# Optimization experiments

Measured on AMD Instinct MI355X. Metric: run time of the kernel, lower is better.

The kernel has to match this reference:

```python
import jax, jax.numpy as jnp
import numpy as np

EPS = 1e-5
NUM_HEADS = 8

def _inorm(x):
    # InstanceNorm1d (affine=False): normalize over last (length) axis per (B, C)
    m = x.mean(axis=-1, keepdims=True)
    v = x.var(axis=-1, keepdims=True)  # biased variance, as torch instance norm
    return (x - m) * jax.lax.rsqrt(v + EPS)

def setup_inputs() -> dict:
    key = jax.random.key(0)
    ks = jax.random.split(key, 12)
    B, Nl, HW = 4, 1024, 4096
    Cl, Cv, Ck, Cval, Cout = 512, 512, 256, 256, 256
    w = lambda k, shape: (jax.random.normal(k, shape, jnp.float32) * 0.02)
    return {
        "l": jax.random.normal(ks[0], (B, Nl, Cl), jnp.float32),
        "x": jax.random.normal(ks[1], (B, HW, Cv), jnp.float32),
        "Wq": w(ks[2], (Ck, Cl)),   "bq": w(ks[3], (Ck,)),
        "Wk": w(ks[4], (Ck, Cv)),   "bk": w(ks[5], (Ck,)),
        "Wv": w(ks[6], (Cval, Cv)), "bv": w(ks[7], (Cval,)),
        "Ww": w(ks[8], (Cout, Cval)), "bw": w(ks[9], (Cout,)),
    }

def reference(l, x, Wq, bq, Wk, bk, Wv, bv, Ww, bw):
    H = NUM_HEADS
    Ck = Wq.shape[0]
    Cv = Wv.shape[0]
    dk, dv = Ck // H, Cv // H
    B, Nl, _ = l.shape
    HW = x.shape[1]

    # 1x1 Conv1d == per-position linear
    q = jnp.einsum('blc,kc->blk', l, Wq) + bq                     # [B, Nl, Ck]
    k = jnp.einsum('bnc,kc->bkn', x, Wk) + bk[None, :, None]      # [B, Ck, HW]
    k = _inorm(k)                                                  # InstanceNorm over HW
    v = jnp.einsum('bnc,kc->bkn', x, Wv) + bv[None, :, None]      # [B, Cv, HW]

    q = q.reshape(B, Nl, H, dk).transpose(0, 2, 1, 3)             # [B, H, Nl, dk]
    k = k.reshape(B, H, dk, HW)                                   # [B, H, dk, HW]
    v = v.reshape(B, H, dv, HW)                                   # [B, H, dv, HW]

    sim = jnp.einsum('bhld,bhdn->bhln', q, k) * (Ck ** -0.5)      # [B, H, Nl, HW]
    att = jax.nn.softmax(sim, axis=-1)
    out = jnp.einsum('bhln,bhdn->bhld', att, v)                   # [B, H, Nl, dv]

    out = out.transpose(0, 2, 1, 3).reshape(B, Nl, Cv)            # [B, Nl, Cv]
    out = jnp.einsum('blc,oc->bol', out, Ww) + bw[None, :, None]  # [B, Cout, Nl]
    out = _inorm(out)                                              # InstanceNorm over Nl
    return out.transpose(0, 2, 1)                                  # [B, Nl, Cout]
```

## Files before the change

kernel.cpp:

```cpp
#include <hip/hip_runtime.h>

constexpr int Bn = 4, NL = 1024, HWn = 4096, NH = 8;

typedef __attribute__((ext_vector_type(8))) short bf16x8;
typedef __attribute__((ext_vector_type(4))) float f32x4;
#define MFMA16 __builtin_amdgcn_mfma_f32_16x16x32_bf16

extern "C" __device__ float __ocml_native_exp2_f32(float);

__device__ __forceinline__ float b2f(unsigned short u) {
  union { unsigned int i; float f; } x; x.i = ((unsigned int)u) << 16; return x.f;
}
__device__ __forceinline__ unsigned short f2b(float f) {
  union { float f; unsigned int i; } x; x.f = f;
  unsigned int r = x.i + 0x7fffu + ((x.i >> 16) & 1u);
  return (unsigned short)(r >> 16);
}

__device__ __forceinline__ void async_load16(const unsigned short* g, unsigned short* l) {
  __builtin_amdgcn_global_load_lds(
      (const __attribute__((address_space(1))) unsigned int*)g,
      (__attribute__((address_space(3))) unsigned int*)l, 16, 0, 0);
}

__global__ __launch_bounds__(256) void conv_bf16(const float* __restrict__ src,
    unsigned short* __restrict__ dst, int n)
{
  int i = (blockIdx.x * 256 + threadIdx.x) * 4;
  if (i < n) {
    float4 v = *(const float4*)(src + i);
    ushort4 o; o.x = f2b(v.x); o.y = f2b(v.y); o.z = f2b(v.z); o.w = f2b(v.w);
    *(ushort4*)(dst + i) = o;
  }
}

__global__ __launch_bounds__(256) void conv_w4(const float* __restrict__ Wk,
    const float* __restrict__ Wv, const float* __restrict__ Wq,
    const float* __restrict__ Ww,
    unsigned short* __restrict__ wkb, unsigned short* __restrict__ wvb,
    unsigned short* __restrict__ wqb,
    unsigned short* __restrict__ wwh, unsigned short* __restrict__ wwl)
{
  int i = (blockIdx.x * 256 + threadIdx.x) * 4;
  if (blockIdx.y == 3) {
    if (i >= 65536) return;
    float4 v = *(const float4*)(Ww + i);
    ushort4 hi, lo;
    hi.x = f2b(v.x); lo.x = f2b(v.x - b2f(hi.x));
    hi.y = f2b(v.y); lo.y = f2b(v.y - b2f(hi.y));
    hi.z = f2b(v.z); lo.z = f2b(v.z - b2f(hi.z));
    hi.w = f2b(v.w); lo.w = f2b(v.w - b2f(hi.w));
    *(ushort4*)(wwh + i) = hi;
    *(ushort4*)(wwl + i) = lo;
    return;
  }
  const float* src = blockIdx.y == 0 ? Wk : (blockIdx.y == 1 ? Wv : Wq);
  unsigned short* dst = blockIdx.y == 0 ? wkb : (blockIdx.y == 1 ? wvb : wqb);
  float4 v = *(const float4*)(src + i);
  ushort4 o; o.x = f2b(v.x); o.y = f2b(v.y); o.z = f2b(v.z); o.w = f2b(v.w);
  *(ushort4*)(dst + i) = o;
}

__global__ __launch_bounds__(256, 3) void gemm128(
    const unsigned short* __restrict__ xbf, const unsigned short* __restrict__ lbf,
    const unsigned short* __restrict__ wkb, const unsigned short* __restrict__ wvb,
    const unsigned short* __restrict__ wqb,
    const float* __restrict__ bk, const float* __restrict__ bv, const float* __restrict__ bq,
    unsigned short* __restrict__ khb, unsigned short* __restrict__ vhb,
    unsigned short* __restrict__ qbuf,
    float* __restrict__ ksum, float* __restrict__ kss, float* __restrict__ vcs)
{
  __shared__ unsigned short As[2][4096];
  __shared__ unsigned short Bs[2][4096];
  const int id = blockIdx.x;
  const int mode = id < 256 ? 0 : (id < 512 ? 1 : 2);
  const int local = id - (mode == 0 ? 0 : (mode == 1 ? 256 : 512));
  const int rb = local >> 1, cb = local & 1;
  const int m0 = rb * 128, n0 = cb * 128;
  const unsigned short* A = (mode == 2) ? lbf : xbf;
  const unsigned short* W = (mode == 0) ? wkb : (mode == 1 ? wvb : wqb);
  const float* bias = (mode == 0) ? bk : (mode == 1 ? bv : bq);

  const int tid = threadIdx.x, w = tid >> 6, lane = tid & 63;
  const int quad = lane >> 4, l15 = lane & 15;
  const int wr = w >> 1, wc = w & 1;

  const int p0 = tid, p1 = tid + 256;
  const int am0 = p0 >> 2, ak0 = (p0 & 3) * 8;
  const int am1 = p1 >> 2, ak1 = (p1 & 3) * 8;

  f32x4 acc[4][4];
#pragma unroll
  for (int i = 0; i < 4; ++i)
#pragma unroll
    for (int j = 0; j < 4; ++j) acc[i][j] = (f32x4){0.f, 0.f, 0.f, 0.f};

  async_load16(A + (size_t)(m0 + am0) * 512 + ak0, &As[0][p0 * 8]);
  async_load16(A + (size_t)(m0 + am1) * 512 + ak1, &As[0][p1 * 8]);
  async_load16(W + (size_t)(n0 + am0) * 512 + ak0, &Bs[0][p0 * 8]);
  async_load16(W + (size_t)(n0 + am1) * 512 + ak1, &Bs[0][p1 * 8]);

  for (int kt = 0; kt < 16; ++kt) {
    const int cur = kt & 1;
    __syncthreads();
    if (kt < 15) {
      int k0 = (kt + 1) * 32;
      async_load16(A + (size_t)(m0 + am0) * 512 + k0 + ak0, &As[cur ^ 1][p0 * 8]);
      async_load16(A + (size_t)(m0 + am1) * 512 + k0 + ak1, &As[cur ^ 1][p1 * 8]);
      async_load16(W + (size_t)(n0 + am0) * 512 + k0 + ak0, &Bs[cur ^ 1][p0 * 8]);
      async_load16(W + (size_t)(n0 + am1) * 512 + k0 + ak1, &Bs[cur ^ 1][p1 * 8]);
    }
    bf16x8 af[4], bf[4];
#pragma unroll
    for (int fr = 0; fr < 4; ++fr)
      af[fr] = *(const bf16x8*)&As[cur][(wr * 64 + fr * 16 + l15) * 32 + quad * 8];
#pragma unroll
    for (int fc = 0; fc < 4; ++fc)
      bf[fc] = *(const bf16x8*)&Bs[cur][(wc * 64 + fc * 16 + l15) * 32 + quad * 8];
#pragma unroll
    for (int fr = 0; fr < 4; ++fr)
#pragma unroll
      for (int fc = 0; fc < 4; ++fc)
        acc[fr][fc] = MFMA16(af[fr], bf[fc], acc[fr][fc], 0, 0, 0);
  }

  float bb[4];
#pragma unroll
  for (int fc = 0; fc < 4; ++fc) bb[fc] = bias[n0 + wc * 64 + fc * 16 + l15];

  if (mode != 2) {
    const int b = m0 >> 12;
    const int seg = (m0 & 4095) >> 9;
#pragma unroll
    for (int fc = 0; fc < 4; ++fc) {
      float s = 0.f, ssq = 0.f;
#pragma unroll
      for (int fr = 0; fr < 4; ++fr)
#pragma unroll
        for (int r = 0; r < 4; ++r) {
          float v = acc[fr][fc][r] + bb[fc];
          s += v; ssq += v * v;
        }
      s += __shfl_xor(s, 16); s += __shfl_xor(s, 32);
      if (mode == 0) {
        ssq += __shfl_xor(ssq, 16); ssq += __shfl_xor(ssq, 32);
        if (quad == 0) {
          int col = n0 + wc * 64 + fc * 16 + l15;
          atomicAdd(&ksum[b * 256 + col], s);
          atomicAdd(&kss[b * 256 + col], ssq);
        }
      } else if (quad == 0) {
        int col = n0 + wc * 64 + fc * 16 + l15;
        atomicAdd(&vcs[seg * 1024 + b * 256 + col], s);
      }
    }
  }

  unsigned short* dst = (mode == 0) ? khb : (mode == 1 ? vhb : qbuf);
#pragma unroll
  for (int fr = 0; fr < 4; ++fr) {
#pragma unroll
    for (int fc = 0; fc < 4; ++fc) {
      int col = n0 + wc * 64 + fc * 16 + l15;
#pragma unroll
      for (int r = 0; r < 4; ++r) {
        int row = m0 + wr * 64 + fr * 16 + quad * 4 + r;
        unsigned short val = f2b(acc[fr][fc][r] + bb[fc]);
        if (mode == 2) {
          dst[(size_t)row * 256 + col] = val;
        } else {
          int b = row >> 12, n = row & 4095, h = col >> 5, d = col & 31;
          dst[((size_t)(b * 8 + h) * 4096 + n) * 32 + d] = val;
        }
      }
    }
  }
}

__global__ __launch_bounds__(256) void kfinal(const float* __restrict__ ksum,
    const float* __restrict__ kss, float* __restrict__ krstd)
{
  int i = blockIdx.x * 256 + threadIdx.x;
  float m = ksum[i] * (1.f / 4096.f);
  float var = kss[i] * (1.f / 4096.f) - m * m;
  krstd[i] = rsqrtf(var + 1e-5f);
}

__global__ __launch_bounds__(256) void vpack(const unsigned short* __restrict__ vh,
    unsigned short* __restrict__ vfrag)
{
  __shared__ unsigned short vt[256][42];
  const int bh = blockIdx.x >> 4, slab = blockIdx.x & 15;
  const unsigned short* src = vh + ((size_t)bh * 4096 + slab * 256) * 32;
  const int t = threadIdx.x;
#pragma unroll
  for (int i = 0; i < 4; ++i) {
    int p = i * 256 + t;
    int n = p >> 2, piece = p & 3;
    uint4 v = *(const uint4*)(src + (size_t)n * 32 + piece * 8);
    unsigned int* lrow = (unsigned int*)&vt[n][piece * 8];
    lrow[0] = v.x; lrow[1] = v.y; lrow[2] = v.z; lrow[3] = v.w;
  }
  __syncthreads();
#pragma unroll
  for (int i = 0; i < 4; ++i) {
    int op = i * 256 + t;
    int lanep = op & 63, rest = op >> 6;
    int dvt = rest & 1, kh2 = (rest >> 1) & 1, chunkl = rest >> 2;
    int lq = lanep >> 4, ll = lanep & 15;
    unsigned short o[8];
#pragma unroll
    for (int j = 0; j < 8; ++j) {
      int kappa = kh2 * 32 + lq * 8 + j;
      int nloc = (kappa >> 2) + 16 * (kappa & 3);
      o[j] = vt[chunkl * 64 + nloc][dvt * 16 + ll];
    }
    size_t dst = ((((size_t)bh * 64 + slab * 4 + chunkl) * 2 + kh2) * 2 + dvt) * 512 + lanep * 8;
    *(bf16x8*)(vfrag + dst) = *(const bf16x8*)o;
  }
}

__global__ __launch_bounds__(256, 4) void attn8(const unsigned short* __restrict__ qbuf,
    const unsigned short* __restrict__ khb, const unsigned short* __restrict__ vfrag,
    const float* __restrict__ krstd, const float* __restrict__ vcs,
    float* __restrict__ po, float* __restrict__ pd)
{
  const int bh = blockIdx.x, b = bh >> 3, h = bh & 7;
  const int lsuper = blockIdx.y, quarter = blockIdx.z;
  const int tid = threadIdx.x, w = tid >> 6, lane = tid & 63;
  const int quad = lane >> 4, l15 = lane & 15;

  __shared__ unsigned short kb_s[2][2048];
  __shared__ unsigned short vb_s[2][2048];
  __shared__ unsigned short ps[4][2][16][64];

  bf16x8 qa[2];
  {
    float fold[8];
    const float* rp = krstd + bh * 32 + quad * 8;
#pragma unroll
    for (int j = 0; j < 8; ++j) fold[j] = rp[j] * (0.0625f * 1.44269504f);
#pragma unroll
    for (int lf = 0; lf < 2; ++lf) {
      int l = lsuper * 128 + w * 32 + lf * 16 + l15;
      bf16x8 qr = *(const bf16x8*)(qbuf + ((size_t)(b * NL + l)) * 256 + h * 32 + quad * 8);
      const unsigned short* qq = (const unsigned short*)&qr;
      unsigned short tmp[8];
#pragma unroll
      for (int j = 0; j < 8; ++j) tmp[j] = f2b(b2f(qq[j]) * fold[j]);
      qa[lf] = *(const bf16x8*)tmp;
    }
  }

  float drow[2][4];
  f32x4 acc[2][2];
#pragma unroll
  for (int lf = 0; lf < 2; ++lf) {
#pragma unroll
    for (int r = 0; r < 4; ++r) drow[lf][r] = 0.f;
    acc[lf][0] = (f32x4){0.f,0.f,0.f,0.f};
    acc[lf][1] = (f32x4){0.f,0.f,0.f,0.f};
  }

  const unsigned short* kcbase = khb + (size_t)bh * 131072 + (size_t)quarter * 1024 * 32;
  const unsigned short* vcbase = vfrag + (size_t)bh * 131072 + (size_t)quarter * 16 * 2048;

  async_load16(kcbase + tid * 8, &kb_s[0][tid * 8]);
  async_load16(vcbase + tid * 8, &vb_s[0][tid * 8]);

  unsigned short* psw = &ps[w][0][0][0];
  const unsigned rdswz = (unsigned)((l15 & 7) << 4);

  for (int c = 0; c < 16; ++c) {
    const int cur = c & 1;
    __syncthreads();
    if (c < 15) {
      async_load16(kcbase + (c + 1) * 2048 + tid * 8, &kb_s[cur ^ 1][tid * 8]);
      async_load16(vcbase + (c + 1) * 2048 + tid * 8, &vb_s[cur ^ 1][tid * 8]);
    }

    bf16x8 kb[4];
#pragma unroll
    for (int t = 0; t < 4; ++t)
      kb[t] = *(const bf16x8*)&kb_s[cur][(t * 16 + l15) * 32 + quad * 8];
    bf16x8 vb[4];
#pragma unroll
    for (int i = 0; i < 4; ++i)
      vb[i] = *(const bf16x8*)&vb_s[cur][i * 512 + lane * 8];

    const f32x4 z = (f32x4){0.f,0.f,0.f,0.f};
#pragma unroll
    for (int lf = 0; lf < 2; ++lf) {
      f32x4 sv[4];
#pragma unroll
      for (int t = 0; t < 4; ++t) sv[t] = MFMA16(qa[lf], kb[t], z, 0, 0, 0);
#pragma unroll
      for (int r = 0; r < 4; ++r) {
        float x0 = __ocml_native_exp2_f32(sv[0][r]);
        float x1 = __ocml_native_exp2_f32(sv[1][r]);
        float x2 = __ocml_native_exp2_f32(sv[2][r]);
        float x3 = __ocml_native_exp2_f32(sv[3][r]);
        drow[lf][r] += (x0 + x1) + (x2 + x3);
        unsigned pk0, pk1;
        asm("v_cvt_pk_bf16_f32 %0, %1, %2" : "=v"(pk0) : "v"(x0 - 1.0f), "v"(x1 - 1.0f));
        asm("v_cvt_pk_bf16_f32 %0, %1, %2" : "=v"(pk1) : "v"(x2 - 1.0f), "v"(x3 - 1.0f));
        const int row = quad * 4 + r;
        unsigned off = (unsigned)((l15 * 8) ^ ((row & 7) << 4));
        uint2 pk; pk.x = pk0; pk.y = pk1;
        *(uint2*)((char*)(psw + lf * 1024 + row * 64) + off) = pk;
      }
      asm volatile("s_waitcnt lgkmcnt(0)" ::: "memory");
#pragma unroll
      for (int kh2 = 0; kh2 < 2; ++kh2) {
        unsigned off = (unsigned)((kh2 * 64 + quad * 16) ^ rdswz);
        bf16x8 pa = *(const bf16x8*)((const char*)(psw + lf * 1024 + l15 * 64) + off);
        acc[lf][0] = MFMA16(pa, vb[kh2 * 2 + 0], acc[lf][0], 0, 0, 0);
        acc[lf][1] = MFMA16(pa, vb[kh2 * 2 + 1], acc[lf][1], 0, 0, 0);
      }
    }
  }

  const float* vc0 = vcs + (quarter * 2) * 1024 + bh * 32;
  const float* vc1 = vc0 + 1024;
  float cs0 = vc0[l15] + vc1[l15];
  float cs1 = vc0[16 + l15] + vc1[16 + l15];
#pragma unroll
  for (int lf = 0; lf < 2; ++lf)
#pragma unroll
    for (int r = 0; r < 4; ++r) {
      acc[lf][0][r] += cs0;
      acc[lf][1][r] += cs1;
    }

  const size_t PDo = (size_t)quarter * 32768 + (size_t)bh * 1024;
#pragma unroll
  for (int lf = 0; lf < 2; ++lf) {
#pragma unroll
    for (int r = 0; r < 4; ++r) {
      float sv = drow[lf][r];
      sv += __shfl_xor(sv, 1, 16);
      sv += __shfl_xor(sv, 2, 16);
      sv += __shfl_xor(sv, 4, 16);
      sv += __shfl_xor(sv, 8, 16);
      int l = lsuper * 128 + w * 32 + lf * 16 + quad * 4 + r;
      float2 val; val.x = acc[lf][0][r]; val.y = acc[lf][1][r];
      *(float2*)(po + (PDo + l) * 32 + l15 * 2) = val;
      if (l15 == 0) pd[PDo + l] = sv;
    }
  }
}

__global__ __launch_bounds__(256) void combine4(const float* __restrict__ po,
    const float* __restrict__ pd, unsigned short* __restrict__ aoh,
    unsigned short* __restrict__ aol)
{
  int gid = blockIdx.x * 256 + threadIdx.x;
  int dv = gid & 31, l = (gid >> 5) & (NL - 1), h = (gid >> 15) & 7, b = gid >> 18;
  int c = ((dv & 15) << 1) | (dv >> 4);
  size_t r = ((size_t)(b * 8 + h)) * 1024 + l;
  float d = 0.f, o = 0.f;
#pragma unroll
  for (int q = 0; q < 4; ++q) {
    size_t rr = (size_t)q * 32768 + r;
    d += pd[rr];
    o += po[rr * 32 + c];
  }
  o = o / d;
  unsigned short hi = f2b(o);
  size_t idx = ((size_t)(b * NL) + l) * 256 + h * 32 + dv;
  aoh[idx] = hi;
  aol[idx] = f2b(o - b2f(hi));
}

__global__ __launch_bounds__(256) void gemm_proj(
    const unsigned short* __restrict__ aoh, const unsigned short* __restrict__ aol,
    const unsigned short* __restrict__ wwh, const unsigned short* __restrict__ wwl,
    const float* __restrict__ bw, float* __restrict__ pj,
    float* __restrict__ psum, float* __restrict__ psq)
{
  __shared__ unsigned short As[64 * 32];
  __shared__ unsigned short Bs[128 * 32];
  const int bm = blockIdx.x * 64, bn = blockIdx.y * 128;
  const int tid = threadIdx.x, w = tid >> 6, lane = tid & 63;
  const int quad = lane >> 4, l15 = lane & 15;
  const int wr = w >> 1, wc = w & 1;
  const int arow = tid >> 2, apiece = (tid & 3) * 8;

  f32x4 acc[2][4];
#pragma unroll
  for (int i = 0; i < 2; ++i)
#pragma unroll
    for (int j = 0; j < 4; ++j) acc[i][j] = (f32x4){0.f, 0.f, 0.f, 0.f};

  for (int pair = 0; pair < 3; ++pair) {
    const unsigned short* A = (pair == 1) ? aol : aoh;
    const unsigned short* Bm = (pair == 2) ? wwl : wwh;
    for (int kt = 0; kt < 8; ++kt) {
      int k0 = kt * 32;
      __syncthreads();
      *(bf16x8*)&As[tid * 8] = *(const bf16x8*)(A + (size_t)(bm + arow) * 256 + k0 + apiece);
#pragma unroll
      for (int it = 0; it < 2; ++it) {
        int p = tid + it * 256;
        int brow = p >> 2, bpiece = (p & 3) * 8;
        *(bf16x8*)&Bs[p * 8] = *(const bf16x8*)(Bm + (size_t)(bn + brow) * 256 + k0 + bpiece);
      }
      __syncthreads();
      bf16x8 af[2], bf[4];
#pragma unroll
      for (int fr = 0; fr < 2; ++fr)
        af[fr] = *(const bf16x8*)&As[(wr * 32 + fr * 16 + l15) * 32 + quad * 8];
#pragma unroll
      for (int fc = 0; fc < 4; ++fc)
        bf[fc] = *(const bf16x8*)&Bs[(wc * 64 + fc * 16 + l15) * 32 + quad * 8];
#pragma unroll
      for (int fr = 0; fr < 2; ++fr)
#pragma unroll
        for (int fc = 0; fc < 4; ++fc)
          acc[fr][fc] = MFMA16(af[fr], bf[fc], acc[fr][fc], 0, 0, 0);
    }
  }

  const int b = bm >> 10;
#pragma unroll
  for (int fr = 0; fr < 2; ++fr)
#pragma unroll
    for (int fc = 0; fc < 4; ++fc) {
      int col = bn + wc * 64 + fc * 16 + l15;
      float bb = bw[col];
      float s = 0.f, ssq = 0.f;
#pragma unroll
      for (int r = 0; r < 4; ++r) {
        int row = bm + wr * 32 + fr * 16 + quad * 4 + r;
        float v = acc[fr][fc][r] + bb;
        pj[(size_t)row * 256 + col] = v;
        s += v; ssq += v * v;
      }
      s += __shfl_xor(s, 16); s += __shfl_xor(s, 32);
      ssq += __shfl_xor(ssq, 16); ssq += __shfl_xor(ssq, 32);
      if (quad == 0) {
        atomicAdd(&psum[b * 256 + col], s);
        atomicAdd(&psq[b * 256 + col], ssq);
      }
    }
}

__global__ __launch_bounds__(256) void finalize_stats(const float* __restrict__ sum,
    const float* __restrict__ sumsq, float invR,
    float* __restrict__ mean, float* __restrict__ rstd)
{
  int i = blockIdx.x * 256 + threadIdx.x;
  float m = sum[i] * invR;
  float v = sumsq[i] * invR - m * m;
  mean[i] = m;
  rstd[i] = rsqrtf(v + 1e-5f);
}

__global__ __launch_bounds__(256) void final_out(const float* __restrict__ proj,
    const float* __restrict__ mean, const float* __restrict__ rstd,
    float* __restrict__ out)
{
  const int b = blockIdx.x, o = threadIdx.x;
  const int l1 = blockIdx.y * 16;
  const float m = mean[b * 256 + o], r = rstd[b * 256 + o];
  for (int i = 0; i < 16; ++i) {
    size_t idx = ((size_t)(b * NL + l1 + i)) * 256 + o;
    out[idx] = (proj[idx] - m) * r;
  }
}

extern "C" void kernel_launch(void* const* d_in, const int* in_sizes, int n_in,
                              void* d_out, int out_size, void* d_ws, size_t ws_size,
                              hipStream_t stream)
{
  const float* l  = (const float*)d_in[0];
  const float* x  = (const float*)d_in[1];
  const float* Wq = (const float*)d_in[2];
  const float* bq = (const float*)d_in[3];
  const float* Wk = (const float*)d_in[4];
  const float* bk = (const float*)d_in[5];
  const float* Wv = (const float*)d_in[6];
  const float* bv = (const float*)d_in[7];
  const float* Ww = (const float*)d_in[8];
  const float* bw = (const float*)d_in[9];
  float* out = (float*)d_out;

  unsigned short* up = (unsigned short*)d_ws;
  unsigned short* xbf   = up;
  unsigned short* lbf   = xbf   + 8388608;
  unsigned short* wkb   = lbf   + 2097152;
  unsigned short* wvb   = wkb   + 131072;
  unsigned short* wqb   = wvb   + 131072;
  unsigned short* qbuf  = wqb   + 131072;
  unsigned short* khb   = qbuf  + 1048576;
  unsigned short* vhb   = khb   + 4194304;
  unsigned short* vfrag = vhb   + 4194304;
  unsigned short* aoh   = vfrag + 4194304;
  unsigned short* aol   = aoh   + 1048576;
  unsigned short* wwh   = aol   + 1048576;
  unsigned short* wwl   = wwh   + 65536;
  float* F     = (float*)((char*)d_ws + 53477376);
  float* ksum  = F;
  float* kss   = F + 1024;
  float* vcs   = F + 2048;
  float* psum  = F + 10240;
  float* psq   = F + 11264;
  float* krstd = F + 12288;
  float* pmean = F + 13312;
  float* prstd = F + 14336;
  float* po    = F + 15360;
  float* pd    = po + 4194304;
  float* pj    = po;

  hipMemsetAsync(F, 0, 12288 * sizeof(float), stream);

  dim3 blk(256);
  conv_bf16<<<8192, blk, 0, stream>>>(x,  xbf, 8388608);
  conv_bf16<<<2048, blk, 0, stream>>>(l,  lbf, 2097152);
  conv_w4<<<dim3(128, 4), blk, 0, stream>>>(Wk, Wv, Wq, Ww, wkb, wvb, wqb, wwh, wwl);
  gemm128<<<576, blk, 0, stream>>>(xbf, lbf, wkb, wvb, wqb, bk, bv, bq,
                                   khb, vhb, qbuf, ksum, kss, vcs);
  kfinal<<<4, blk, 0, stream>>>(ksum, kss, krstd);
  vpack<<<512, blk, 0, stream>>>(vhb, vfrag);
  attn8<<<dim3(32, 8, 4), blk, 0, stream>>>(qbuf, khb, vfrag, krstd, vcs, po, pd);
  combine4<<<4096, blk, 0, stream>>>(po, pd, aoh, aol);
  gemm_proj<<<dim3(64, 2), blk, 0, stream>>>(aoh, aol, wwh, wwl, bw, pj, psum, psq);
  finalize_stats<<<4, blk, 0, stream>>>(psum, psq, 1.0f / NL, pmean, prstd);
  final_out<<<dim3(4, 64), blk, 0, stream>>>(pj, pmean, prstd, out);
}
```

Baseline: 191.4 us.

## Merge conversion kernels and memset, inline stat finalization, retile projection GEMM

```diff
diff --git a/kernel.cpp b/kernel.cpp
--- a/kernel.cpp
+++ b/kernel.cpp
@@ -23,42 +23,52 @@
       (__attribute__((address_space(3))) unsigned int*)l, 16, 0, 0);
 }
 
-__global__ __launch_bounds__(256) void conv_bf16(const float* __restrict__ src,
-    unsigned short* __restrict__ dst, int n)
-{
-  int i = (blockIdx.x * 256 + threadIdx.x) * 4;
-  if (i < n) {
+__global__ __launch_bounds__(256) void convall(const float* __restrict__ x,
+    const float* __restrict__ l,
+    const float* __restrict__ Wk, const float* __restrict__ Wv,
+    const float* __restrict__ Wq, const float* __restrict__ Ww,
+    unsigned short* __restrict__ xbf, unsigned short* __restrict__ lbf,
+    unsigned short* __restrict__ wkb, unsigned short* __restrict__ wvb,
+    unsigned short* __restrict__ wqb,
+    unsigned short* __restrict__ wwh, unsigned short* __restrict__ wwl,
+    float* __restrict__ Fz)
+{
+  const int id = blockIdx.x, tid = threadIdx.x;
+  if (id < 8192) {
+    int i = (id * 256 + tid) * 4;
+    float4 v = *(const float4*)(x + i);
+    ushort4 o; o.x = f2b(v.x); o.y = f2b(v.y); o.z = f2b(v.z); o.w = f2b(v.w);
+    *(ushort4*)(xbf + i) = o;
+  } else if (id < 10240) {
+    int i = ((id - 8192) * 256 + tid) * 4;
+    float4 v = *(const float4*)(l + i);
+    ushort4 o; o.x = f2b(v.x); o.y = f2b(v.y); o.z = f2b(v.z); o.w = f2b(v.w);
+    *(ushort4*)(lbf + i) = o;
+  } else if (id < 10752) {
+    int sub = id - 10240;
+    int y = sub >> 7, bx = sub & 127;
+    int i = (bx * 256 + tid) * 4;
+    if (y == 3) {
+      if (i >= 65536) return;
+      float4 v = *(const float4*)(Ww + i);
+      ushort4 hi, lo;
+      hi.x = f2b(v.x); lo.x = f2b(v.x - b2f(hi.x));
+      hi.y = f2b(v.y); lo.y = f2b(v.y - b2f(hi.y));
+      hi.z = f2b(v.z); lo.z = f2b(v.z - b2f(hi.z));
+      hi.w = f2b(v.w); lo.w = f2b(v.w - b2f(hi.w));
+      *(ushort4*)(wwh + i) = hi;
+      *(ushort4*)(wwl + i) = lo;
+      return;
+    }
+    const float* src = y == 0 ? Wk : (y == 1 ? Wv : Wq);
+    unsigned short* dst = y == 0 ? wkb : (y == 1 ? wvb : wqb);
     float4 v = *(const float4*)(src + i);
     ushort4 o; o.x = f2b(v.x); o.y = f2b(v.y); o.z = f2b(v.z); o.w = f2b(v.w);
     *(ushort4*)(dst + i) = o;
-  }
-}
-
-__global__ __launch_bounds__(256) void conv_w4(const float* __restrict__ Wk,
-    const float* __restrict__ Wv, const float* __restrict__ Wq,
-    const float* __restrict__ Ww,
-    unsigned short* __restrict__ wkb, unsigned short* __restrict__ wvb,
-    unsigned short* __restrict__ wqb,
-    unsigned short* __restrict__ wwh, unsigned short* __restrict__ wwl)
-{
-  int i = (blockIdx.x * 256 + threadIdx.x) * 4;
-  if (blockIdx.y == 3) {
-    if (i >= 65536) return;
-    float4 v = *(const float4*)(Ww + i);
-    ushort4 hi, lo;
-    hi.x = f2b(v.x); lo.x = f2b(v.x - b2f(hi.x));
-    hi.y = f2b(v.y); lo.y = f2b(v.y - b2f(hi.y));
-    hi.z = f2b(v.z); lo.z = f2b(v.z - b2f(hi.z));
-    hi.w = f2b(v.w); lo.w = f2b(v.w - b2f(hi.w));
-    *(ushort4*)(wwh + i) = hi;
-    *(ushort4*)(wwl + i) = lo;
-    return;
-  }
-  const float* src = blockIdx.y == 0 ? Wk : (blockIdx.y == 1 ? Wv : Wq);
-  unsigned short* dst = blockIdx.y == 0 ? wkb : (blockIdx.y == 1 ? wvb : wqb);
-  float4 v = *(const float4*)(src + i);
-  ushort4 o; o.x = f2b(v.x); o.y = f2b(v.y); o.z = f2b(v.z); o.w = f2b(v.w);
-  *(ushort4*)(dst + i) = o;
+  } else {
+    int i = (id - 10752) * 1024 + tid * 4;
+    *(float4*)(Fz + i) = (float4){0.f, 0.f, 0.f, 0.f};
+  }
 }
 
 __global__ __launch_bounds__(256, 3) void gemm128(
@@ -177,15 +187,6 @@
   }
 }
 
-__global__ __launch_bounds__(256) void kfinal(const float* __restrict__ ksum,
-    const float* __restrict__ kss, float* __restrict__ krstd)
-{
-  int i = blockIdx.x * 256 + threadIdx.x;
-  float m = ksum[i] * (1.f / 4096.f);
-  float var = kss[i] * (1.f / 4096.f) - m * m;
-  krstd[i] = rsqrtf(var + 1e-5f);
-}
-
 __global__ __launch_bounds__(256) void vpack(const unsigned short* __restrict__ vh,
     unsigned short* __restrict__ vfrag)
 {
@@ -222,7 +223,8 @@
 
 __global__ __launch_bounds__(256, 4) void attn8(const unsigned short* __restrict__ qbuf,
     const unsigned short* __restrict__ khb, const unsigned short* __restrict__ vfrag,
-    const float* __restrict__ krstd, const float* __restrict__ vcs,
+    const float* __restrict__ ksum, const float* __restrict__ kss,
+    const float* __restrict__ vcs,
     float* __restrict__ po, float* __restrict__ pd)
 {
   const int bh = blockIdx.x, b = bh >> 3, h = bh & 7;
@@ -237,9 +239,13 @@
   bf16x8 qa[2];
   {
     float fold[8];
-    const float* rp = krstd + bh * 32 + quad * 8;
-#pragma unroll
-    for (int j = 0; j < 8; ++j) fold[j] = rp[j] * (0.0625f * 1.44269504f);
+    const int ch = bh * 32 + quad * 8;
+#pragma unroll
+    for (int j = 0; j < 8; ++j) {
+      float m = ksum[ch + j] * (1.f / 4096.f);
+      float var = kss[ch + j] * (1.f / 4096.f) - m * m;
+      fold[j] = rsqrtf(var + 1e-5f) * (0.0625f * 1.44269504f);
+    }
 #pragma unroll
     for (int lf = 0; lf < 2; ++lf) {
       int l = lsuper * 128 + w * 32 + lf * 16 + l15;
@@ -379,18 +385,18 @@
     float* __restrict__ psum, float* __restrict__ psq)
 {
   __shared__ unsigned short As[64 * 32];
-  __shared__ unsigned short Bs[128 * 32];
-  const int bm = blockIdx.x * 64, bn = blockIdx.y * 128;
+  __shared__ unsigned short Bs[64 * 32];
+  const int bm = blockIdx.x * 64, bn = blockIdx.y * 64;
   const int tid = threadIdx.x, w = tid >> 6, lane = tid & 63;
   const int quad = lane >> 4, l15 = lane & 15;
   const int wr = w >> 1, wc = w & 1;
   const int arow = tid >> 2, apiece = (tid & 3) * 8;
 
-  f32x4 acc[2][4];
+  f32x4 acc[2][2];
 #pragma unroll
   for (int i = 0; i < 2; ++i)
 #pragma unroll
-    for (int j = 0; j < 4; ++j) acc[i][j] = (f32x4){0.f, 0.f, 0.f, 0.f};
+    for (int j = 0; j < 2; ++j) acc[i][j] = (f32x4){0.f, 0.f, 0.f, 0.f};
 
   for (int pair = 0; pair < 3; ++pair) {
     const unsigned short* A = (pair == 1) ? aol : aoh;
@@ -399,24 +405,19 @@
       int k0 = kt * 32;
       __syncthreads();
       *(bf16x8*)&As[tid * 8] = *(const bf16x8*)(A + (size_t)(bm + arow) * 256 + k0 + apiece);
-#pragma unroll
-      for (int it = 0; it < 2; ++it) {
-        int p = tid + it * 256;
-        int brow = p >> 2, bpiece = (p & 3) * 8;
-        *(bf16x8*)&Bs[p * 8] = *(const bf16x8*)(Bm + (size_t)(bn + brow) * 256 + k0 + bpiece);
-      }
+      *(bf16x8*)&Bs[tid * 8] = *(const bf16x8*)(Bm + (size_t)(bn + arow) * 256 + k0 + apiece);
       __syncthreads();
-      bf16x8 af[2], bf[4];
+      bf16x8 af[2], bf[2];
 #pragma unroll
       for (int fr = 0; fr < 2; ++fr)
         af[fr] = *(const bf16x8*)&As[(wr * 32 + fr * 16 + l15) * 32 + quad * 8];
 #pragma unroll
-      for (int fc = 0; fc < 4; ++fc)
-        bf[fc] = *(const bf16x8*)&Bs[(wc * 64 + fc * 16 + l15) * 32 + quad * 8];
+      for (int fc = 0; fc < 2; ++fc)
+        bf[fc] = *(const bf16x8*)&Bs[(wc * 32 + fc * 16 + l15) * 32 + quad * 8];
 #pragma unroll
       for (int fr = 0; fr < 2; ++fr)
 #pragma unroll
-        for (int fc = 0; fc < 4; ++fc)
+        for (int fc = 0; fc < 2; ++fc)
           acc[fr][fc] = MFMA16(af[fr], bf[fc], acc[fr][fc], 0, 0, 0);
     }
   }
@@ -425,8 +426,8 @@
 #pragma unroll
   for (int fr = 0; fr < 2; ++fr)
 #pragma unroll
-    for (int fc = 0; fc < 4; ++fc) {
-      int col = bn + wc * 64 + fc * 16 + l15;
+    for (int fc = 0; fc < 2; ++fc) {
+      int col = bn + wc * 32 + fc * 16 + l15;
       float bb = bw[col];
       float s = 0.f, ssq = 0.f;
 #pragma unroll
@@ -445,24 +446,14 @@
     }
 }
 
-__global__ __launch_bounds__(256) void finalize_stats(const float* __restrict__ sum,
-    const float* __restrict__ sumsq, float invR,
-    float* __restrict__ mean, float* __restrict__ rstd)
-{
-  int i = blockIdx.x * 256 + threadIdx.x;
-  float m = sum[i] * invR;
-  float v = sumsq[i] * invR - m * m;
-  mean[i] = m;
-  rstd[i] = rsqrtf(v + 1e-5f);
-}
-
 __global__ __launch_bounds__(256) void final_out(const float* __restrict__ proj,
-    const float* __restrict__ mean, const float* __restrict__ rstd,
+    const float* __restrict__ psum, const float* __restrict__ psq,
     float* __restrict__ out)
 {
   const int b = blockIdx.x, o = threadIdx.x;
   const int l1 = blockIdx.y * 16;
-  const float m = mean[b * 256 + o], r = rstd[b * 256 + o];
+  const float m = psum[b * 256 + o] * (1.f / 1024.f);
+  const float r = rsqrtf(psq[b * 256 + o] * (1.f / 1024.f) - m * m + 1e-5f);
   for (int i = 0; i < 16; ++i) {
     size_t idx = ((size_t)(b * NL + l1 + i)) * 256 + o;
     out[idx] = (proj[idx] - m) * r;
@@ -505,26 +496,18 @@
   float* vcs   = F + 2048;
   float* psum  = F + 10240;
   float* psq   = F + 11264;
-  float* krstd = F + 12288;
-  float* pmean = F + 13312;
-  float* prstd = F + 14336;
   float* po    = F + 15360;
   float* pd    = po + 4194304;
   float* pj    = po;
 
-  hipMemsetAsync(F, 0, 12288 * sizeof(float), stream);
-
   dim3 blk(256);
-  conv_bf16<<<8192, blk, 0, stream>>>(x,  xbf, 8388608);
-  conv_bf16<<<2048, blk, 0, stream>>>(l,  lbf, 2097152);
-  conv_w4<<<dim3(128, 4), blk, 0, stream>>>(Wk, Wv, Wq, Ww, wkb, wvb, wqb, wwh, wwl);
+  convall<<<10764, blk, 0, stream>>>(x, l, Wk, Wv, Wq, Ww, xbf, lbf,
+                                     wkb, wvb, wqb, wwh, wwl, F);
   gemm128<<<576, blk, 0, stream>>>(xbf, lbf, wkb, wvb, wqb, bk, bv, bq,
                                    khb, vhb, qbuf, ksum, kss, vcs);
-  kfinal<<<4, blk, 0, stream>>>(ksum, kss, krstd);
   vpack<<<512, blk, 0, stream>>>(vhb, vfrag);
-  attn8<<<dim3(32, 8, 4), blk, 0, stream>>>(qbuf, khb, vfrag, krstd, vcs, po, pd);
+  attn8<<<dim3(32, 8, 4), blk, 0, stream>>>(qbuf, khb, vfrag, ksum, kss, vcs, po, pd);
   combine4<<<4096, blk, 0, stream>>>(po, pd, aoh, aol);
-  gemm_proj<<<dim3(64, 2), blk, 0, stream>>>(aoh, aol, wwh, wwl, bw, pj, psum, psq);
-  finalize_stats<<<4, blk, 0, stream>>>(psum, psq, 1.0f / NL, pmean, prstd);
-  final_out<<<dim3(4, 64), blk, 0, stream>>>(pj, pmean, prstd, out);
-}
+  gemm_proj<<<dim3(64, 4), blk, 0, stream>>>(aoh, aol, wwh, wwl, bw, pj, psum, psq);
+  final_out<<<dim3(4, 64), blk, 0, stream>>>(pj, psum, psq, out);
+}
```

After: 179.7 us. 1.07x faster.
